# Optimization experiments

Measured on AMD Instinct MI355X. Metric: run time of the kernel, lower is better.

Reference implementation:

```python
import jax, jax.numpy as jnp
import numpy as np

# Model dims (match init_kwargs)
L, H, CV, NRBF = 4, 64, 16, 16   # layers, scalar hidden, vector channels (hidden/channels_div analog), radial basis size
HEADS, DH = 8, 8                 # num_heads, head dim (H // HEADS)
K = 32                           # k nearest neighbors
DIN = H + H + NRBF + CV + CV     # invariant edge-feature width = 176
N_ATOM_TYPES, ATOM_DIM, TIME_DIM, N_T = 32, 32, 32, 1000


def _sinusoidal(seq_len, dim):
    pos = np.arange(seq_len, dtype=np.float32)[:, None]
    dims = np.arange(dim, dtype=np.float32)[None, :]
    ang = pos / 10000 ** (2 * np.floor(dims / 2) / dim)
    emb = np.zeros((seq_len, dim), np.float32)
    emb[:, 0::2] = np.sin(ang[:, 0::2])
    emb[:, 1::2] = np.cos(ang[:, 1::2])
    return jnp.asarray(emb)


def _knn_idx(coord, k):
    # coord [b,n,3]; squared distances via gram trick (no [b,n,n,3] intermediate)
    sq = jnp.sum(coord * coord, axis=-1)
    d2 = sq[:, :, None] + sq[:, None, :] - 2.0 * jnp.einsum('bnd,bmd->bnm', coord, coord)
    n = coord.shape[1]
    d2 = d2 + jnp.eye(n, dtype=coord.dtype) * 1e9  # exclude self-loops
    _, idx = jax.lax.top_k(-d2, k)
    return idx  # [b,n,k] source-node indices for each destination node


_gather = jax.vmap(lambda x, i: x[i])  # ([n,...],[n,k]) -> [n,k,...], vmapped over batch


def _rbf(d, rmax=10.0):
    mu = jnp.linspace(0.0, rmax, NRBF)
    sigma = rmax / NRBF
    return jnp.exp(-((d[..., None] - mu) ** 2) / (2.0 * sigma * sigma))


def setup_inputs():
    key = jax.random.key(0)
    ks = jax.random.split(key, 16)
    b, n = 2, 2048

    def w(k, shape, scale):
        return jax.random.normal(k, shape, jnp.float32) * scale

    s = 1.0 / np.sqrt(H)
    return {
        'sequence': jax.random.randint(ks[0], (b, n), 0, N_ATOM_TYPES),
        'coordinate': jax.random.normal(ks[1], (b, n, 3), jnp.float32) * 3.0,
        't': 500,
        'atom_table': w(ks[2], (N_ATOM_TYPES, ATOM_DIM), 1.0),
        'time_table': _sinusoidal(N_T, TIME_DIM),
        'Wp0': w(ks[3], (ATOM_DIM + TIME_DIM, H), 1.0 / np.sqrt(ATOM_DIM + TIME_DIM)),
        'bp0': jnp.zeros((H,), jnp.float32),
        'Wp1': w(ks[4], (CV,), 1.0),
        'We1': w(ks[5], (L, DIN, H), 1.0 / np.sqrt(DIN)),
        'be1': jnp.zeros((L, H), jnp.float32),
        'We2': w(ks[6], (L, H, H), s),
        'be2': jnp.zeros((L, H), jnp.float32),
        'Wq': w(ks[7], (L, H, H), s),
        'Wk': w(ks[8], (L, H, H), s),
        'Wv0': w(ks[9], (L, H, H), s),
        'Wv1': w(ks[10], (L, H, CV), s),
        'Wg1': w(ks[11], (L, H, CV), s),
        'Wo0': w(ks[12], (L, H, H), s),
        'bo0': jnp.zeros((L, H), jnp.float32),
        'Wout1': w(ks[13], (CV,), 1.0 / np.sqrt(CV)),
    }


def reference(sequence, coordinate, t, atom_table, time_table, Wp0, bp0, Wp1,
              We1, be1, We2, be2, Wq, Wk, Wv0, Wv1, Wg1, Wo0, bo0, Wout1):
    b, n, _ = coordinate.shape
    coord = coordinate - jnp.mean(coordinate, axis=1, keepdims=True)

    # KNN graph + per-edge relative positions (src - dst), dense [b,n,K] layout
    idx = _knn_idx(coord, K)
    rel = _gather(coord, idx) - coord[:, :, None, :]      # [b,n,K,3]
    d = jnp.sqrt(jnp.sum(rel * rel, axis=-1) + 1e-8)
    dirn = rel / d[..., None]                             # degree-1 spherical harmonic direction
    rbf = _rbf(d)                                         # [b,n,K,NRBF]

    # input fibers: degree-0 = atom embedding ++ timestep embedding; degree-1 = coordinates
    f0 = jnp.concatenate([atom_table[sequence],
                          jnp.broadcast_to(time_table[t], (b, n, TIME_DIM))], axis=-1)
    f0 = f0 @ Wp0 + bp0                                   # [b,n,H]
    f1 = coord[:, :, None, :] * Wp1[None, None, :, None]  # [b,n,CV,3]

    for l in range(L):
        f0s = _gather(f0, idx)                            # [b,n,K,H] source scalars
        f1s = _gather(f1, idx)                            # [b,n,K,CV,3] source vectors
        dot_s = jnp.einsum('bnkcd,bnkd->bnkc', f1s, dirn) # invariants <f1_src, dir>
        dot_d = jnp.einsum('bncd,bnkd->bnkc', f1, dirn)   # invariants <f1_dst, dir>
        e = jnp.concatenate([jnp.broadcast_to(f0[:, :, None, :], f0s.shape),
                             f0s, rbf, dot_s, dot_d], axis=-1)
        m = jax.nn.relu(e @ We1[l] + be1[l]) @ We2[l] + be2[l]   # [b,n,K,H]

        # multi-head attention over the K neighbors
        q = (f0 @ Wq[l]).reshape(b, n, HEADS, DH)
        kk = (m @ Wk[l]).reshape(b, n, K, HEADS, DH)
        logits = jnp.einsum('bnhd,bnkhd->bnkh', q, kk) / np.sqrt(DH)
        attn = jax.nn.softmax(logits, axis=2)

        v0 = (m @ Wv0[l]).reshape(b, n, K, HEADS, DH)
        agg0 = jnp.einsum('bnkh,bnkhd->bnhd', attn, v0).reshape(b, n, H)
        f0 = f0 + agg0 @ Wo0[l] + bo0[l]

        # equivariant degree-1 update: dir-outer-product + gated source vectors
        a = attn.mean(axis=-1)                            # [b,n,K]
        v1 = dirn[..., None, :] * (m @ Wv1[l])[..., None] + (m @ Wg1[l])[..., None] * f1s
        f1 = f1 + jnp.einsum('bnk,bnkcd->bncd', a, v1)

    # output fiber: single degree-1 channel -> updated coordinates
    return jnp.einsum('bncd,c->bnd', f1, Wout1)           # [b,n,3]
```

## Files before the change

### kernel.cpp

```cpp
#include <hip/hip_runtime.h>
#include <hip/hip_bf16.h>
#include <math.h>

#define NL    4
#define H     64
#define CV    16
#define NRBF  16
#define HEADS 8
#define KK    32
#define DIN   176
#define NB    2
#define NN    2048
#define F1W   (CV*3)
#define NTILES 136

typedef __attribute__((ext_vector_type(8))) short short8v;
typedef __attribute__((ext_vector_type(4))) float floatx4;

__device__ __forceinline__ ushort f2bf(float f) {
  union { float f; unsigned u; } v; v.f = f;
  unsigned r = v.u + 0x7FFFu + ((v.u >> 16) & 1u);
  return (ushort)(r >> 16);
}
__device__ __forceinline__ float bf2f(ushort s) {
  union { unsigned u; float f; } v; v.u = ((unsigned)s) << 16;
  return v.f;
}
__device__ __forceinline__ void split_bf(float v, ushort& h, ushort& l) {
  h = f2bf(v);
  l = f2bf(v - bf2f(h));
}
__device__ __forceinline__ floatx4 mfma3(short8v ah, short8v al,
                                         short8v bh, short8v bl, floatx4 acc) {
  acc = __builtin_amdgcn_mfma_f32_16x16x32_bf16(ah, bh, acc, 0, 0, 0);
  acc = __builtin_amdgcn_mfma_f32_16x16x32_bf16(ah, bl, acc, 0, 0, 0);
  acc = __builtin_amdgcn_mfma_f32_16x16x32_bf16(al, bh, acc, 0, 0, 0);
  return acc;
}

__global__ __launch_bounds__(256) void k_center(const float* __restrict__ coord,
                                                float* __restrict__ coordC) {
  __shared__ float rx[256], ry[256], rz[256];
  int b = blockIdx.x;
  const float* cb = coord + b*NN*3;
  float sx = 0.f, sy = 0.f, sz = 0.f;
  for (int i = threadIdx.x; i < NN; i += 256) {
    sx += cb[i*3+0]; sy += cb[i*3+1]; sz += cb[i*3+2];
  }
  rx[threadIdx.x] = sx; ry[threadIdx.x] = sy; rz[threadIdx.x] = sz;
  __syncthreads();
  for (int s = 128; s > 0; s >>= 1) {
    if (threadIdx.x < s) {
      rx[threadIdx.x] += rx[threadIdx.x+s];
      ry[threadIdx.x] += ry[threadIdx.x+s];
      rz[threadIdx.x] += rz[threadIdx.x+s];
    }
    __syncthreads();
  }
  float mx = rx[0]*(1.0f/NN), my = ry[0]*(1.0f/NN), mz = rz[0]*(1.0f/NN);
  float* ob = coordC + b*NN*3;
  for (int i = threadIdx.x; i < NN; i += 256) {
    ob[i*3+0] = cb[i*3+0] - mx;
    ob[i*3+1] = cb[i*3+1] - my;
    ob[i*3+2] = cb[i*3+2] - mz;
  }
}

__global__ __launch_bounds__(64) void k_knn(const float* __restrict__ coordC,
                                            int* __restrict__ idx,
                                            float* __restrict__ dirn,
                                            ushort* __restrict__ rbf16) {
  __shared__ unsigned long long heap[64*33];
  const int node = blockIdx.x;
  const int b = node >> 11;
  const int i = node & (NN-1);
  const int l = threadIdx.x;
  const float* cb = coordC + b*NN*3;
  const float xi = cb[i*3+0], yi = cb[i*3+1], zi = cb[i*3+2];
  const float sqi = xi*xi + yi*yi + zi*zi;
  unsigned long long key[32];
  #pragma unroll
  for (int it = 0; it < 32; ++it) {
    int j = it*64 + l;
    float xj = cb[j*3+0], yj = cb[j*3+1], zj = cb[j*3+2];
    float sqj = xj*xj + yj*yj + zj*zj;
    float dot = xi*xj + yi*yj + zi*zj;
    float v = sqi + sqj - 2.0f*dot;
    if (j == i) v += 1.0e9f;
    unsigned u = __float_as_uint(v);
    u ^= (u >> 31) ? 0xFFFFFFFFu : 0x80000000u;
    key[it] = (((unsigned long long)u) << 16) | (unsigned)j;
  }
  #pragma unroll
  for (int k2 = 2; k2 <= 32; k2 <<= 1) {
    #pragma unroll
    for (int jj = k2 >> 1; jj > 0; jj >>= 1) {
      #pragma unroll
      for (int ii = 0; ii < 32; ++ii) {
        int ixj = ii ^ jj;
        if (ixj > ii) {
          bool up = ((ii & k2) == 0);
          unsigned long long a = key[ii], c = key[ixj];
          bool sw = (a > c) == up;
          unsigned long long lo = sw ? c : a;
          unsigned long long hi = sw ? a : c;
          key[ii] = lo; key[ixj] = hi;
        }
      }
    }
  }
  unsigned long long* row = heap + l*33;
  #pragma unroll
  for (int it = 0; it < 32; ++it) row[it] = key[it];
  row[32] = 0xFFFFFFFFFFFFFFFFULL;
  int ptr = 0;
  unsigned long long head = key[0];
  int myselidx = 0;
  for (int s = 0; s < KK; ++s) {
    unsigned long long w = head;
    #pragma unroll
    for (int off = 1; off <= 32; off <<= 1) {
      unsigned long long o = __shfl_xor(w, off, 64);
      w = (o < w) ? o : w;
    }
    int wj = (int)(w & 0xFFFFull);
    if (l == s) myselidx = wj;
    if ((wj & 63) == l) { ++ptr; head = row[ptr]; }
  }
  if (l < KK) {
    int j = myselidx;
    idx[node*KK + l] = j;
    float rxv = cb[j*3+0] - xi, ryv = cb[j*3+1] - yi, rzv = cb[j*3+2] - zi;
    float dd = sqrtf(rxv*rxv + ryv*ryv + rzv*rzv + 1e-8f);
    float inv = 1.0f/dd;
    float* dn = dirn + (node*KK + l)*3;
    dn[0] = rxv*inv; dn[1] = ryv*inv; dn[2] = rzv*inv;
    ushort* rb = rbf16 + (size_t)(node*KK + l)*NRBF;
    const float inv2s2 = 1.0f/(2.0f*0.625f*0.625f);
    #pragma unroll
    for (int r = 0; r < NRBF; ++r) {
      float mu = (10.0f/15.0f)*(float)r;
      float dm = dd - mu;
      rb[r] = f2bf(expf(-(dm*dm)*inv2s2));
    }
  }
}

__global__ __launch_bounds__(256) void k_f0init(const int* __restrict__ seq,
                                                const int* __restrict__ tptr,
                                                const float* __restrict__ atab,
                                                const float* __restrict__ ttab,
                                                const float* __restrict__ Wp0,
                                                const float* __restrict__ bp0,
                                                float* __restrict__ f0) {
  int gidx = blockIdx.x*256 + threadIdx.x;
  int node = gidx >> 6, o = gidx & (H-1);
  int s = seq[node];
  int tv = tptr[0];
  const float* ar = atab + s*32;
  const float* tr = ttab + tv*32;
  float acc = bp0[o];
  for (int i2 = 0; i2 < 32; ++i2) acc = fmaf(ar[i2], Wp0[i2*H + o], acc);
  for (int i2 = 0; i2 < 32; ++i2) acc = fmaf(tr[i2], Wp0[(32+i2)*H + o], acc);
  f0[gidx] = acc;
}

__global__ __launch_bounds__(256) void k_f1init(const float* __restrict__ coordC,
                                                const float* __restrict__ Wp1,
                                                float* __restrict__ f1) {
  int gidx = blockIdx.x*256 + threadIdx.x;
  if (gidx >= NB*NN*F1W) return;
  int node = gidx / F1W;
  int r = gidx - node*F1W;
  int c = r / 3, d = r - c*3;
  f1[gidx] = coordC[node*3 + d] * Wp1[c];
}

__global__ __launch_bounds__(256) void k_prep(
    const float* __restrict__ We1, const float* __restrict__ We2,
    const float* __restrict__ Wq,  const float* __restrict__ Wk,
    const float* __restrict__ Wv0, const float* __restrict__ Wv1,
    const float* __restrict__ Wg1, const float* __restrict__ Wo0,
    ushort* __restrict__ wfrag) {
  int gid = blockIdx.x*256 + threadIdx.x;
  if (gid >= NL*NTILES*64) return;
  int lane = gid & 63;
  int tile = gid >> 6;
  int l = tile / NTILES;
  int tt = tile - l*NTILES;
  int part = (tt >= 68) ? 1 : 0;
  int t = part ? (tt - 68) : tt;
  int kt, nt, K = H;
  const float* src = nullptr;
  int wvg = 0;
  if (t < 24)      { kt = t>>2;           nt = t&3; src = We1 + (size_t)l*DIN*H; K = DIN; }
  else if (t < 32) { int u=t-24; kt=u>>2; nt = u&3; src = We2 + (size_t)l*H*H; }
  else if (t < 40) { int u=t-32; kt=u>>2; nt = u&3; src = Wk  + (size_t)l*H*H; }
  else if (t < 48) { int u=t-40; kt=u>>2; nt = u&3; src = Wq  + (size_t)l*H*H; }
  else if (t < 56) { int u=t-48; kt=u>>2; nt = u&3; src = Wv0 + (size_t)l*H*H; }
  else if (t < 60) { int u=t-56; kt=u>>1; nt = u&1; wvg = 1; }
  else             { int u=t-60; kt=u>>2; nt = u&3; src = Wo0 + (size_t)l*H*H; }
  ushort out[8];
  #pragma unroll
  for (int j = 0; j < 8; ++j) {
    int k = kt*32 + (lane>>4)*8 + j;
    int col = nt*16 + (lane&15);
    float v = 0.f;
    if (k < K) {
      if (wvg) v = (col < CV) ? Wv1[(size_t)l*H*CV + k*CV + col]
                              : Wg1[(size_t)l*H*CV + k*CV + (col-CV)];
      else     v = src[(size_t)k*H + col];
    }
    ushort h, lo; split_bf(v, h, lo);
    out[j] = part ? lo : h;
  }
  *(short8v*)(wfrag + (size_t)tile*512 + lane*8) = *(const short8v*)out;
}

__global__ __launch_bounds__(128) void k_layer(
    const float* __restrict__ f0i, const float* __restrict__ f1i,
    float* __restrict__ f0o, float* __restrict__ f1o,
    const int* __restrict__ idx, const float* __restrict__ dirn,
    const ushort* __restrict__ rbf16,
    const ushort* __restrict__ wfl,
    const float* __restrict__ be1, const float* __restrict__ be2,
    const float* __restrict__ bo0)
{
  __shared__ __align__(16) ushort regionA  [32*72];
  __shared__ __align__(16) ushort regionAlo[32*72];
  __shared__ __align__(16) ushort regionB  [32*72];
  __shared__ __align__(16) ushort regionBlo[32*72];
  __shared__ __align__(16) ushort sF0h[64], sF0l[64];
  __shared__ __align__(16) ushort sAggH[64], sAggL[64];
  __shared__ float sF1d[F1W];
  __shared__ float sDir[KK][4];
  __shared__ int   sIdx[KK];
  __shared__ float sAtt[KK*9];
  __shared__ float sA[KK];
  __shared__ float sQ[64];
  __shared__ float sAggP[2][64];

  const int t    = threadIdx.x;
  const int wid  = t >> 6;
  const int lane = t & 63;
  const int node = blockIdx.x;
  const int bbase = node & ~(NN-1);
  const int r0 = lane & 15, g = lane >> 4;
  const int mrow = wid*16 + r0;
  const floatx4 fz = {0.f, 0.f, 0.f, 0.f};

  short8v cbh[4], cbl[4];
  #pragma unroll
  for (int nt = 0; nt < 4; ++nt) {
    cbh[nt] = *(const short8v*)&wfl[(size_t)(nt)*512 + lane*8];
    cbl[nt] = *(const short8v*)&wfl[(size_t)(68 + nt)*512 + lane*8];
  }

  float f0reg = 0.f;
  if (wid == 0) {
    f0reg = f0i[node*H + lane];
    ushort h, l; split_bf(f0reg, h, l); sF0h[lane] = h; sF0l[lane] = l;
  } else {
    if (lane < KK)  sIdx[lane] = idx[node*KK + lane];
    if (lane < F1W) sF1d[lane] = f1i[node*F1W + lane];
  }
  if (t < 96) sDir[t/3][t%3] = dirn[node*(KK*3) + t];
  __syncthreads();

  #pragma unroll 4
  for (int r = 0; r < 16; ++r) {
    int rr = wid*16 + r;
    float v = f0i[(bbase + sIdx[rr])*H + lane];
    ushort h, l; split_bf(v, h, l);
    regionA[rr*72 + lane] = h; regionAlo[rr*72 + lane] = l;
  }
  #pragma unroll
  for (int it = 0; it < 4; ++it) {
    int q = it*64 + lane;
    int k = wid*16 + (q >> 4), c = q & 15;
    regionB  [k*72 + c] = rbf16[(size_t)node*(KK*NRBF) + k*NRBF + c];
    regionBlo[k*72 + c] = 0;
    regionB  [k*72 + 48 + c] = 0;
    regionBlo[k*72 + 48 + c] = 0;
  }
  #pragma unroll
  for (int it = 0; it < 4; ++it) {
    int q = it*64 + lane;
    int k = wid*16 + (q >> 4), ch = q & 15;
    const float* fs = f1i + (size_t)(bbase + sIdx[k])*F1W + ch*3;
    float ds_ = 0.f, dd_ = 0.f;
    #pragma unroll
    for (int d = 0; d < 3; ++d) {
      float dr = sDir[k][d];
      ds_ += fs[d] * dr;
      dd_ += sF1d[ch*3 + d] * dr;
    }
    ushort h, l;
    split_bf(ds_, h, l); regionB[k*72 + 16 + ch] = h; regionBlo[k*72 + 16 + ch] = l;
    split_bf(dd_, h, l); regionB[k*72 + 32 + ch] = h; regionBlo[k*72 + 32 + ch] = l;
  }

  floatx4 c1[4];
  #pragma unroll
  for (int nt = 0; nt < 4; ++nt) c1[nt] = fz;
  #pragma unroll
  for (int kt = 0; kt < 6; ++kt) {
    short8v nbh[4], nbl[4];
    if (kt < 5) {
      #pragma unroll
      for (int nt = 0; nt < 4; ++nt) {
        nbh[nt] = *(const short8v*)&wfl[(size_t)((kt+1)*4 + nt)*512 + lane*8];
        nbl[nt] = *(const short8v*)&wfl[(size_t)(68 + (kt+1)*4 + nt)*512 + lane*8];
      }
    }
    short8v ah, al;
    if (kt < 2) {
      ah = *(const short8v*)&sF0h[kt*32 + g*8];
      al = *(const short8v*)&sF0l[kt*32 + g*8];
    } else if (kt < 4) {
      int off = (kt-2)*32 + g*8;
      ah = *(const short8v*)&regionA  [mrow*72 + off];
      al = *(const short8v*)&regionAlo[mrow*72 + off];
    } else {
      int off = ((kt == 4) ? 0 : 32) + g*8;
      ah = *(const short8v*)&regionB  [mrow*72 + off];
      al = *(const short8v*)&regionBlo[mrow*72 + off];
    }
    #pragma unroll
    for (int nt = 0; nt < 4; ++nt) c1[nt] = mfma3(ah, al, cbh[nt], cbl[nt], c1[nt]);
    if (kt < 5) {
      #pragma unroll
      for (int nt = 0; nt < 4; ++nt) { cbh[nt] = nbh[nt]; cbl[nt] = nbl[nt]; }
    }
  }
  short8v b2h[8], b2l[8];
  #pragma unroll
  for (int i2 = 0; i2 < 8; ++i2) {
    b2h[i2] = *(const short8v*)&wfl[(size_t)(24 + i2)*512 + lane*8];
    b2l[i2] = *(const short8v*)&wfl[(size_t)(92 + i2)*512 + lane*8];
  }
  #pragma unroll
  for (int nt = 0; nt < 4; ++nt) {
    float be = be1[nt*16 + r0];
    #pragma unroll
    for (int i = 0; i < 4; ++i) {
      float v = fmaxf(c1[nt][i] + be, 0.f);
      ushort h, l; split_bf(v, h, l);
      regionA  [(wid*16 + g*4 + i)*72 + nt*16 + r0] = h;
      regionAlo[(wid*16 + g*4 + i)*72 + nt*16 + r0] = l;
    }
  }

  floatx4 c2[4];
  #pragma unroll
  for (int nt = 0; nt < 4; ++nt) c2[nt] = fz;
  #pragma unroll
  for (int kt = 0; kt < 2; ++kt) {
    int off = kt*32 + g*8;
    short8v ah = *(const short8v*)&regionA  [mrow*72 + off];
    short8v al = *(const short8v*)&regionAlo[mrow*72 + off];
    #pragma unroll
    for (int nt = 0; nt < 4; ++nt)
      c2[nt] = mfma3(ah, al, b2h[kt*4 + nt], b2l[kt*4 + nt], c2[nt]);
  }
  #pragma unroll
  for (int nt = 0; nt < 4; ++nt) {
    float be = be2[nt*16 + r0];
    #pragma unroll
    for (int i = 0; i < 4; ++i) {
      ushort h, l; split_bf(c2[nt][i] + be, h, l);
      regionB  [(wid*16 + g*4 + i)*72 + nt*16 + r0] = h;
      regionBlo[(wid*16 + g*4 + i)*72 + nt*16 + r0] = l;
    }
  }

  floatx4 ck[4];
  #pragma unroll
  for (int nt = 0; nt < 4; ++nt) ck[nt] = fz;
  if (wid == 0) {
    floatx4 cq[4];
    #pragma unroll
    for (int nt = 0; nt < 4; ++nt) cq[nt] = fz;
    #pragma unroll
    for (int kt = 0; kt < 2; ++kt) {
      short8v ah = *(const short8v*)&sF0h[kt*32 + g*8];
      short8v al = *(const short8v*)&sF0l[kt*32 + g*8];
      #pragma unroll
      for (int nt = 0; nt < 4; ++nt) {
        short8v bh = *(const short8v*)&wfl[(size_t)(40 + kt*4 + nt)*512 + lane*8];
        short8v bl = *(const short8v*)&wfl[(size_t)(108 + kt*4 + nt)*512 + lane*8];
        cq[nt] = mfma3(ah, al, bh, bl, cq[nt]);
      }
    }
    if (g == 0) {
      #pragma unroll
      for (int nt = 0; nt < 4; ++nt) sQ[nt*16 + r0] = cq[nt][0];
    }
  } else {
    #pragma unroll
    for (int kt = 0; kt < 2; ++kt) {
      int off = kt*32 + g*8;
      short8v ah = *(const short8v*)&regionB  [mrow*72 + off];
      short8v al = *(const short8v*)&regionBlo[mrow*72 + off];
      #pragma unroll
      for (int nt = 0; nt < 4; ++nt) {
        short8v bh = *(const short8v*)&wfl[(size_t)(32 + kt*4 + nt)*512 + lane*8];
        short8v bl = *(const short8v*)&wfl[(size_t)(100 + kt*4 + nt)*512 + lane*8];
        ck[nt] = mfma3(ah, al, bh, bl, ck[nt]);
      }
    }
  }
  __syncthreads();

  floatx4 cv[4];
  #pragma unroll
  for (int nt = 0; nt < 4; ++nt) cv[nt] = fz;
  if (wid == 0) {
    #pragma unroll
    for (int kt = 0; kt < 2; ++kt) {
      int off = kt*32 + g*8;
      short8v ah = *(const short8v*)&regionB  [mrow*72 + off];
      short8v al = *(const short8v*)&regionBlo[mrow*72 + off];
      #pragma unroll
      for (int nt = 0; nt < 4; ++nt) {
        short8v bh = *(const short8v*)&wfl[(size_t)(32 + kt*4 + nt)*512 + lane*8];
        short8v bl = *(const short8v*)&wfl[(size_t)(100 + kt*4 + nt)*512 + lane*8];
        ck[nt] = mfma3(ah, al, bh, bl, ck[nt]);
      }
    }
  } else {
    #pragma unroll
    for (int kt = 0; kt < 2; ++kt) {
      int off = kt*32 + g*8;
      short8v ah = *(const short8v*)&regionB  [mrow*72 + off];
      short8v al = *(const short8v*)&regionBlo[mrow*72 + off];
      #pragma unroll
      for (int nt = 0; nt < 4; ++nt) {
        short8v bh = *(const short8v*)&wfl[(size_t)(48 + kt*4 + nt)*512 + lane*8];
        short8v bl = *(const short8v*)&wfl[(size_t)(116 + kt*4 + nt)*512 + lane*8];
        cv[nt] = mfma3(ah, al, bh, bl, cv[nt]);
      }
    }
  }
  {
    float qv[4];
    #pragma unroll
    for (int nt = 0; nt < 4; ++nt) qv[nt] = sQ[nt*16 + r0];
    #pragma unroll
    for (int nt = 0; nt < 4; ++nt)
      #pragma unroll
      for (int i = 0; i < 4; ++i) {
        float v = ck[nt][i] * qv[nt];
        v += __shfl_xor(v, 1, 64);
        v += __shfl_xor(v, 2, 64);
        v += __shfl_xor(v, 4, 64);
        if ((lane & 7) == 0)
          sAtt[(wid*16 + g*4 + i)*9 + nt*2 + (r0 >> 3)] = v * 0.35355339059327373f;
      }
  }
  __syncthreads();

  floatx4 cvg[2];
  cvg[0] = fz; cvg[1] = fz;
  if (wid == 1) {
    int h = lane & 7, seg = lane >> 3;
    float l0[4];
    float mx = -3.0e38f;
    #pragma unroll
    for (int i = 0; i < 4; ++i) { l0[i] = sAtt[(seg*4 + i)*9 + h]; mx = fmaxf(mx, l0[i]); }
    #pragma unroll
    for (int off = 8; off <= 32; off <<= 1) mx = fmaxf(mx, __shfl_xor(mx, off, 64));
    float e0[4], sum = 0.f;
    #pragma unroll
    for (int i = 0; i < 4; ++i) { e0[i] = expf(l0[i] - mx); sum += e0[i]; }
    #pragma unroll
    for (int off = 8; off <= 32; off <<= 1) sum += __shfl_xor(sum, off, 64);
    float inv = 1.0f / sum;
    #pragma unroll
    for (int i = 0; i < 4; ++i) {
      float a = e0[i] * inv;
      sAtt[(seg*4 + i)*9 + h] = a;
      float tt = a;
      tt += __shfl_xor(tt, 1, 64);
      tt += __shfl_xor(tt, 2, 64);
      tt += __shfl_xor(tt, 4, 64);
      if (h == 0) sA[seg*4 + i] = tt * 0.125f;
    }
  } else {
    #pragma unroll
    for (int kt = 0; kt < 2; ++kt) {
      int off = kt*32 + g*8;
      short8v ah = *(const short8v*)&regionB  [mrow*72 + off];
      short8v al = *(const short8v*)&regionBlo[mrow*72 + off];
      #pragma unroll
      for (int nt = 0; nt < 4; ++nt) {
        short8v bh = *(const short8v*)&wfl[(size_t)(48 + kt*4 + nt)*512 + lane*8];
        short8v bl = *(const short8v*)&wfl[(size_t)(116 + kt*4 + nt)*512 + lane*8];
        cv[nt] = mfma3(ah, al, bh, bl, cv[nt]);
      }
      #pragma unroll
      for (int nt = 0; nt < 2; ++nt) {
        short8v bh = *(const short8v*)&wfl[(size_t)(56 + kt*2 + nt)*512 + lane*8];
        short8v bl = *(const short8v*)&wfl[(size_t)(124 + kt*2 + nt)*512 + lane*8];
        cvg[nt] = mfma3(ah, al, bh, bl, cvg[nt]);
      }
    }
    float* sMvg = (float*)regionA;
    #pragma unroll
    for (int nt = 0; nt < 2; ++nt)
      #pragma unroll
      for (int i = 0; i < 4; ++i)
        sMvg[(g*4 + i)*34 + nt*16 + r0] = cvg[nt][i];
  }
  __syncthreads();

  short8v b7h[8], b7l[8];
  if (wid == 0) {
    #pragma unroll
    for (int i2 = 0; i2 < 8; ++i2) {
      b7h[i2] = *(const short8v*)&wfl[(size_t)(60 + i2)*512 + lane*8];
      b7l[i2] = *(const short8v*)&wfl[(size_t)(128 + i2)*512 + lane*8];
    }
  }
  {
    int hsub = r0 >> 3;
    #pragma unroll
    for (int nt = 0; nt < 4; ++nt) {
      float p = 0.f;
      #pragma unroll
      for (int i = 0; i < 4; ++i)
        p += sAtt[(wid*16 + g*4 + i)*9 + nt*2 + hsub] * cv[nt][i];
      p += __shfl_xor(p, 16, 64);
      p += __shfl_xor(p, 32, 64);
      if (g == 0) sAggP[wid][nt*16 + r0] = p;
    }
  }
  if (wid == 1) {
    cvg[0] = fz; cvg[1] = fz;
    #pragma unroll
    for (int kt = 0; kt < 2; ++kt) {
      int off = kt*32 + g*8;
      short8v ah = *(const short8v*)&regionB  [mrow*72 + off];
      short8v al = *(const short8v*)&regionBlo[mrow*72 + off];
      #pragma unroll
      for (int nt = 0; nt < 2; ++nt) {
        short8v bh = *(const short8v*)&wfl[(size_t)(56 + kt*2 + nt)*512 + lane*8];
        short8v bl = *(const short8v*)&wfl[(size_t)(124 + kt*2 + nt)*512 + lane*8];
        cvg[nt] = mfma3(ah, al, bh, bl, cvg[nt]);
      }
    }
    float* sMvg = (float*)regionA;
    #pragma unroll
    for (int nt = 0; nt < 2; ++nt)
      #pragma unroll
      for (int i = 0; i < 4; ++i)
        sMvg[(16 + g*4 + i)*34 + nt*16 + r0] = cvg[nt][i];
  }
  __syncthreads();

  if (wid == 0) {
    {
      float p = sAggP[0][lane] + sAggP[1][lane];
      ushort h, l; split_bf(p, h, l);
      sAggH[lane] = h; sAggL[lane] = l;
    }
    floatx4 co[4];
    #pragma unroll
    for (int nt = 0; nt < 4; ++nt) co[nt] = fz;
    #pragma unroll
    for (int kt = 0; kt < 2; ++kt) {
      short8v ah = *(const short8v*)&sAggH[kt*32 + g*8];
      short8v al = *(const short8v*)&sAggL[kt*32 + g*8];
      #pragma unroll
      for (int nt = 0; nt < 4; ++nt)
        co[nt] = mfma3(ah, al, b7h[kt*4 + nt], b7l[kt*4 + nt], co[nt]);
    }
    float v = (g == 0) ? co[0][0] : (g == 1) ? co[1][0] : (g == 2) ? co[2][0] : co[3][0];
    f0o[node*H + lane] = f0reg + v + bo0[lane];
  } else if (lane < F1W) {
    const float* sMvg = (const float*)regionA;
    int ch = lane / 3, d = lane - ch*3;
    float acc = sF1d[lane];
    #pragma unroll 8
    for (int k = 0; k < KK; ++k) {
      float f1s = f1i[(size_t)(bbase + sIdx[k])*F1W + lane];
      float a   = sA[k];
      float mv1 = sMvg[k*34 + ch];
      float mg1 = sMvg[k*34 + 16 + ch];
      acc += a * (sDir[k][d]*mv1 + mg1*f1s);
    }
    f1o[node*F1W + lane] = acc;
  }
}

__global__ __launch_bounds__(256) void k_out(const float* __restrict__ f1,
                                             const float* __restrict__ Wout1,
                                             float* __restrict__ out) {
  int gidx = blockIdx.x*256 + threadIdx.x;
  if (gidx >= NB*NN*3) return;
  int node = gidx / 3, d = gidx - node*3;
  float acc = 0.f;
  for (int c = 0; c < CV; ++c) acc = fmaf(f1[node*F1W + c*3 + d], Wout1[c], acc);
  out[gidx] = acc;
}

extern "C" void kernel_launch(void* const* d_in, const int* in_sizes, int n_in,
                              void* d_out, int out_size, void* d_ws, size_t ws_size,
                              hipStream_t stream) {
  const int*   seq   = (const int*)  d_in[0];
  const float* coord = (const float*)d_in[1];
  const int*   tptr  = (const int*)  d_in[2];
  const float* atab  = (const float*)d_in[3];
  const float* ttab  = (const float*)d_in[4];
  const float* Wp0   = (const float*)d_in[5];
  const float* bp0   = (const float*)d_in[6];
  const float* Wp1   = (const float*)d_in[7];
  const float* We1   = (const float*)d_in[8];
  const float* be1   = (const float*)d_in[9];
  const float* We2   = (const float*)d_in[10];
  const float* be2   = (const float*)d_in[11];
  const float* Wq    = (const float*)d_in[12];
  const float* Wk    = (const float*)d_in[13];
  const float* Wv0   = (const float*)d_in[14];
  const float* Wv1   = (const float*)d_in[15];
  const float* Wg1   = (const float*)d_in[16];
  const float* Wo0   = (const float*)d_in[17];
  const float* bo0   = (const float*)d_in[18];
  const float* Wout1 = (const float*)d_in[19];
  float* out = (float*)d_out;

  float* ws = (float*)d_ws;
  float*  coordC = ws;
  int*    idxb   = (int*)(ws + 12288);
  float*  dirn   = ws + 12288 + 131072;
  float*  f0A    = dirn + (size_t)NB*NN*KK*3;
  float*  f0B    = f0A + (size_t)NB*NN*H;
  float*  f1A    = f0B + (size_t)NB*NN*H;
  float*  f1B    = f1A + (size_t)NB*NN*F1W;
  ushort* rbf16  = (ushort*)(f1B + (size_t)NB*NN*F1W);
  ushort* wfrag  = rbf16 + (size_t)NB*NN*KK*NRBF;

  k_center<<<NB, 256, 0, stream>>>(coord, coordC);
  k_knn<<<NB*NN, 64, 0, stream>>>(coordC, idxb, dirn, rbf16);
  k_f0init<<<NB*NN*H/256, 256, 0, stream>>>(seq, tptr, atab, ttab, Wp0, bp0, f0A);
  k_f1init<<<(NB*NN*F1W + 255)/256, 256, 0, stream>>>(coordC, Wp1, f1A);
  k_prep<<<(NL*NTILES*64 + 255)/256, 256, 0, stream>>>(We1, We2, Wq, Wk, Wv0, Wv1, Wg1, Wo0, wfrag);

  const float* f0in = f0A; float* f0out = f0B;
  const float* f1in = f1A; float* f1out = f1B;
  for (int l = 0; l < NL; ++l) {
    k_layer<<<NB*NN, 128, 0, stream>>>(
        f0in, f1in, f0out, f1out, idxb, dirn, rbf16,
        wfrag + (size_t)l*NTILES*512,
        be1 + (size_t)l*H, be2 + (size_t)l*H, bo0 + (size_t)l*H);
    const float* tf0 = f0in; f0in = f0out; f0out = (float*)tf0;
    const float* tf1 = f1in; f1in = f1out; f1out = (float*)tf1;
  }
  k_out<<<(NB*NN*3 + 255)/256, 256, 0, stream>>>(f1in, Wout1, out);
}
```

Measured before the change: 368.9 us.

## Split per-node layer kernel across four waves with N-split MFMA tiles

Raises k_layer from 128 to 256 threads. Each wave now owns a 16-row M tile and half of the N tiles, so weight fragments are loaded per use instead of being held in registers. Softmax is spread across all waves with per-head 32-lane reductions and a partial-sum array for head-mean attention. The aim is more parallelism per node and lower register pressure. In exchange the kernel adds several extra __syncthreads and reloads weight fragments from global/L2 more often.

```diff
diff --git a/kernel.cpp b/kernel.cpp
--- a/kernel.cpp
+++ b/kernel.cpp
@@ -217,7 +217,7 @@
   *(short8v*)(wfrag + (size_t)tile*512 + lane*8) = *(const short8v*)out;
 }
 
-__global__ __launch_bounds__(128) void k_layer(
+__global__ __launch_bounds__(256, 6) void k_layer(
     const float* __restrict__ f0i, const float* __restrict__ f1i,
     float* __restrict__ f0o, float* __restrict__ f1o,
     const int* __restrict__ idx, const float* __restrict__ dirn,
@@ -239,54 +239,56 @@
   __shared__ float sA[KK];
   __shared__ float sQ[64];
   __shared__ float sAggP[2][64];
+  __shared__ float sAPart[4][32];
 
   const int t    = threadIdx.x;
   const int wid  = t >> 6;
   const int lane = t & 63;
+  const int mt   = wid >> 1;
+  const int nh   = wid & 1;
   const int node = blockIdx.x;
   const int bbase = node & ~(NN-1);
   const int r0 = lane & 15, g = lane >> 4;
-  const int mrow = wid*16 + r0;
+  const int mrow = mt*16 + r0;
   const floatx4 fz = {0.f, 0.f, 0.f, 0.f};
-
-  short8v cbh[4], cbl[4];
-  #pragma unroll
-  for (int nt = 0; nt < 4; ++nt) {
-    cbh[nt] = *(const short8v*)&wfl[(size_t)(nt)*512 + lane*8];
-    cbl[nt] = *(const short8v*)&wfl[(size_t)(68 + nt)*512 + lane*8];
-  }
 
   float f0reg = 0.f;
   if (wid == 0) {
     f0reg = f0i[node*H + lane];
     ushort h, l; split_bf(f0reg, h, l); sF0h[lane] = h; sF0l[lane] = l;
+  } else if (wid == 1) {
+    if (lane < KK) sIdx[lane] = idx[node*KK + lane];
+  } else if (wid == 2) {
+    if (lane < F1W) sF1d[lane] = f1i[node*F1W + lane];
   } else {
-    if (lane < KK)  sIdx[lane] = idx[node*KK + lane];
-    if (lane < F1W) sF1d[lane] = f1i[node*F1W + lane];
-  }
-  if (t < 96) sDir[t/3][t%3] = dirn[node*(KK*3) + t];
-  __syncthreads();
-
-  #pragma unroll 4
-  for (int r = 0; r < 16; ++r) {
-    int rr = wid*16 + r;
+    sDir[lane/3][lane%3] = dirn[node*(KK*3) + lane];
+    if (lane < 32) {
+      int e = 64 + lane;
+      sDir[e/3][e%3] = dirn[node*(KK*3) + e];
+    }
+  }
+  __syncthreads();
+
+  #pragma unroll
+  for (int r = 0; r < 8; ++r) {
+    int rr = wid*8 + r;
     float v = f0i[(bbase + sIdx[rr])*H + lane];
     ushort h, l; split_bf(v, h, l);
     regionA[rr*72 + lane] = h; regionAlo[rr*72 + lane] = l;
   }
   #pragma unroll
-  for (int it = 0; it < 4; ++it) {
-    int q = it*64 + lane;
-    int k = wid*16 + (q >> 4), c = q & 15;
-    regionB  [k*72 + c] = rbf16[(size_t)node*(KK*NRBF) + k*NRBF + c];
+  for (int it = 0; it < 2; ++it) {
+    int p = it*256 + t;
+    int k = p >> 4, c = p & 15;
+    regionB  [k*72 + c] = rbf16[(size_t)node*(KK*NRBF) + p];
     regionBlo[k*72 + c] = 0;
     regionB  [k*72 + 48 + c] = 0;
     regionBlo[k*72 + 48 + c] = 0;
   }
   #pragma unroll
-  for (int it = 0; it < 4; ++it) {
-    int q = it*64 + lane;
-    int k = wid*16 + (q >> 4), ch = q & 15;
+  for (int it = 0; it < 2; ++it) {
+    int p = it*256 + t;
+    int k = p >> 4, ch = p & 15;
     const float* fs = f1i + (size_t)(bbase + sIdx[k])*F1W + ch*3;
     float ds_ = 0.f, dd_ = 0.f;
     #pragma unroll
@@ -299,20 +301,11 @@
     split_bf(ds_, h, l); regionB[k*72 + 16 + ch] = h; regionBlo[k*72 + 16 + ch] = l;
     split_bf(dd_, h, l); regionB[k*72 + 32 + ch] = h; regionBlo[k*72 + 32 + ch] = l;
   }
-
-  floatx4 c1[4];
-  #pragma unroll
-  for (int nt = 0; nt < 4; ++nt) c1[nt] = fz;
+  __syncthreads();
+
+  floatx4 c1[2]; c1[0] = fz; c1[1] = fz;
   #pragma unroll
   for (int kt = 0; kt < 6; ++kt) {
-    short8v nbh[4], nbl[4];
-    if (kt < 5) {
-      #pragma unroll
-      for (int nt = 0; nt < 4; ++nt) {
-        nbh[nt] = *(const short8v*)&wfl[(size_t)((kt+1)*4 + nt)*512 + lane*8];
-        nbl[nt] = *(const short8v*)&wfl[(size_t)(68 + (kt+1)*4 + nt)*512 + lane*8];
-      }
-    }
     short8v ah, al;
     if (kt < 2) {
       ah = *(const short8v*)&sF0h[kt*32 + g*8];
@@ -327,74 +320,87 @@
       al = *(const short8v*)&regionBlo[mrow*72 + off];
     }
     #pragma unroll
-    for (int nt = 0; nt < 4; ++nt) c1[nt] = mfma3(ah, al, cbh[nt], cbl[nt], c1[nt]);
-    if (kt < 5) {
-      #pragma unroll
-      for (int nt = 0; nt < 4; ++nt) { cbh[nt] = nbh[nt]; cbl[nt] = nbl[nt]; }
-    }
-  }
-  short8v b2h[8], b2l[8];
-  #pragma unroll
-  for (int i2 = 0; i2 < 8; ++i2) {
-    b2h[i2] = *(const short8v*)&wfl[(size_t)(24 + i2)*512 + lane*8];
-    b2l[i2] = *(const short8v*)&wfl[(size_t)(92 + i2)*512 + lane*8];
-  }
-  #pragma unroll
-  for (int nt = 0; nt < 4; ++nt) {
-    float be = be1[nt*16 + r0];
+    for (int j = 0; j < 2; ++j) {
+      int ntg = nh*2 + j;
+      short8v bh = *(const short8v*)&wfl[(size_t)(kt*4 + ntg)*512 + lane*8];
+      short8v bl = *(const short8v*)&wfl[(size_t)(68 + kt*4 + ntg)*512 + lane*8];
+      c1[j] = mfma3(ah, al, bh, bl, c1[j]);
+    }
+  }
+  #pragma unroll
+  for (int j = 0; j < 2; ++j) {
+    int ntg = nh*2 + j;
+    float be = be1[ntg*16 + r0];
     #pragma unroll
     for (int i = 0; i < 4; ++i) {
-      float v = fmaxf(c1[nt][i] + be, 0.f);
+      float v = fmaxf(c1[j][i] + be, 0.f);
       ushort h, l; split_bf(v, h, l);
-      regionA  [(wid*16 + g*4 + i)*72 + nt*16 + r0] = h;
-      regionAlo[(wid*16 + g*4 + i)*72 + nt*16 + r0] = l;
-    }
-  }
-
-  floatx4 c2[4];
-  #pragma unroll
-  for (int nt = 0; nt < 4; ++nt) c2[nt] = fz;
+      regionA  [(mt*16 + g*4 + i)*72 + ntg*16 + r0] = h;
+      regionAlo[(mt*16 + g*4 + i)*72 + ntg*16 + r0] = l;
+    }
+  }
+  __syncthreads();
+
+  floatx4 c2[2]; c2[0] = fz; c2[1] = fz;
   #pragma unroll
   for (int kt = 0; kt < 2; ++kt) {
     int off = kt*32 + g*8;
     short8v ah = *(const short8v*)&regionA  [mrow*72 + off];
     short8v al = *(const short8v*)&regionAlo[mrow*72 + off];
     #pragma unroll
-    for (int nt = 0; nt < 4; ++nt)
-      c2[nt] = mfma3(ah, al, b2h[kt*4 + nt], b2l[kt*4 + nt], c2[nt]);
-  }
-  #pragma unroll
-  for (int nt = 0; nt < 4; ++nt) {
-    float be = be2[nt*16 + r0];
+    for (int j = 0; j < 2; ++j) {
+      int ntg = nh*2 + j;
+      short8v bh = *(const short8v*)&wfl[(size_t)(24 + kt*4 + ntg)*512 + lane*8];
+      short8v bl = *(const short8v*)&wfl[(size_t)(92 + kt*4 + ntg)*512 + lane*8];
+      c2[j] = mfma3(ah, al, bh, bl, c2[j]);
+    }
+  }
+  __syncthreads();
+  #pragma unroll
+  for (int j = 0; j < 2; ++j) {
+    int ntg = nh*2 + j;
+    float be = be2[ntg*16 + r0];
     #pragma unroll
     for (int i = 0; i < 4; ++i) {
-      ushort h, l; split_bf(c2[nt][i] + be, h, l);
-      regionB  [(wid*16 + g*4 + i)*72 + nt*16 + r0] = h;
-      regionBlo[(wid*16 + g*4 + i)*72 + nt*16 + r0] = l;
-    }
-  }
-
-  floatx4 ck[4];
-  #pragma unroll
-  for (int nt = 0; nt < 4; ++nt) ck[nt] = fz;
-  if (wid == 0) {
-    floatx4 cq[4];
-    #pragma unroll
-    for (int nt = 0; nt < 4; ++nt) cq[nt] = fz;
+      ushort h, l; split_bf(c2[j][i] + be, h, l);
+      regionB  [(mt*16 + g*4 + i)*72 + ntg*16 + r0] = h;
+      regionBlo[(mt*16 + g*4 + i)*72 + ntg*16 + r0] = l;
+    }
+  }
+  __syncthreads();
+
+  floatx4 ck[2]; ck[0] = fz; ck[1] = fz;
+  floatx4 cv[2]; cv[0] = fz; cv[1] = fz;
+  #pragma unroll
+  for (int kt = 0; kt < 2; ++kt) {
+    int off = kt*32 + g*8;
+    short8v ah = *(const short8v*)&regionB  [mrow*72 + off];
+    short8v al = *(const short8v*)&regionBlo[mrow*72 + off];
+    #pragma unroll
+    for (int j = 0; j < 2; ++j) {
+      int ntg = nh*2 + j;
+      short8v bh = *(const short8v*)&wfl[(size_t)(32 + kt*4 + ntg)*512 + lane*8];
+      short8v bl = *(const short8v*)&wfl[(size_t)(100 + kt*4 + ntg)*512 + lane*8];
+      ck[j] = mfma3(ah, al, bh, bl, ck[j]);
+    }
+  }
+  if (mt == 0) {
+    floatx4 cq[2]; cq[0] = fz; cq[1] = fz;
     #pragma unroll
     for (int kt = 0; kt < 2; ++kt) {
       short8v ah = *(const short8v*)&sF0h[kt*32 + g*8];
       short8v al = *(const short8v*)&sF0l[kt*32 + g*8];
       #pragma unroll
-      for (int nt = 0; nt < 4; ++nt) {
-        short8v bh = *(const short8v*)&wfl[(size_t)(40 + kt*4 + nt)*512 + lane*8];
-        short8v bl = *(const short8v*)&wfl[(size_t)(108 + kt*4 + nt)*512 + lane*8];
-        cq[nt] = mfma3(ah, al, bh, bl, cq[nt]);
+      for (int j = 0; j < 2; ++j) {
+        int ntg = nh*2 + j;
+        short8v bh = *(const short8v*)&wfl[(size_t)(40 + kt*4 + ntg)*512 + lane*8];
+        short8v bl = *(const short8v*)&wfl[(size_t)(108 + kt*4 + ntg)*512 + lane*8];
+        cq[j] = mfma3(ah, al, bh, bl, cq[j]);
       }
     }
     if (g == 0) {
-      #pragma unroll
-      for (int nt = 0; nt < 4; ++nt) sQ[nt*16 + r0] = cq[nt][0];
+      sQ[(nh*2 + 0)*16 + r0] = cq[0][0];
+      sQ[(nh*2 + 1)*16 + r0] = cq[1][0];
     }
   } else {
     #pragma unroll
@@ -403,159 +409,99 @@
       short8v ah = *(const short8v*)&regionB  [mrow*72 + off];
       short8v al = *(const short8v*)&regionBlo[mrow*72 + off];
       #pragma unroll
-      for (int nt = 0; nt < 4; ++nt) {
-        short8v bh = *(const short8v*)&wfl[(size_t)(32 + kt*4 + nt)*512 + lane*8];
-        short8v bl = *(const short8v*)&wfl[(size_t)(100 + kt*4 + nt)*512 + lane*8];
-        ck[nt] = mfma3(ah, al, bh, bl, ck[nt]);
+      for (int j = 0; j < 2; ++j) {
+        int ntg = nh*2 + j;
+        short8v bh = *(const short8v*)&wfl[(size_t)(48 + kt*4 + ntg)*512 + lane*8];
+        short8v bl = *(const short8v*)&wfl[(size_t)(116 + kt*4 + ntg)*512 + lane*8];
+        cv[j] = mfma3(ah, al, bh, bl, cv[j]);
       }
     }
   }
   __syncthreads();
 
-  floatx4 cv[4];
-  #pragma unroll
-  for (int nt = 0; nt < 4; ++nt) cv[nt] = fz;
-  if (wid == 0) {
+  #pragma unroll
+  for (int j = 0; j < 2; ++j) {
+    int ntg = nh*2 + j;
+    float qv = sQ[ntg*16 + r0];
+    #pragma unroll
+    for (int i = 0; i < 4; ++i) {
+      float v = ck[j][i] * qv;
+      v += __shfl_xor(v, 1, 64);
+      v += __shfl_xor(v, 2, 64);
+      v += __shfl_xor(v, 4, 64);
+      if ((lane & 7) == 0)
+        sAtt[(mt*16 + g*4 + i)*9 + ntg*2 + (r0 >> 3)] = v * 0.35355339059327373f;
+    }
+  }
+  if (mt == 0) {
     #pragma unroll
     for (int kt = 0; kt < 2; ++kt) {
       int off = kt*32 + g*8;
       short8v ah = *(const short8v*)&regionB  [mrow*72 + off];
       short8v al = *(const short8v*)&regionBlo[mrow*72 + off];
       #pragma unroll
-      for (int nt = 0; nt < 4; ++nt) {
-        short8v bh = *(const short8v*)&wfl[(size_t)(32 + kt*4 + nt)*512 + lane*8];
-        short8v bl = *(const short8v*)&wfl[(size_t)(100 + kt*4 + nt)*512 + lane*8];
-        ck[nt] = mfma3(ah, al, bh, bl, ck[nt]);
+      for (int j = 0; j < 2; ++j) {
+        int ntg = nh*2 + j;
+        short8v bh = *(const short8v*)&wfl[(size_t)(48 + kt*4 + ntg)*512 + lane*8];
+        short8v bl = *(const short8v*)&wfl[(size_t)(116 + kt*4 + ntg)*512 + lane*8];
+        cv[j] = mfma3(ah, al, bh, bl, cv[j]);
       }
     }
   } else {
-    #pragma unroll
-    for (int kt = 0; kt < 2; ++kt) {
-      int off = kt*32 + g*8;
-      short8v ah = *(const short8v*)&regionB  [mrow*72 + off];
-      short8v al = *(const short8v*)&regionBlo[mrow*72 + off];
-      #pragma unroll
-      for (int nt = 0; nt < 4; ++nt) {
-        short8v bh = *(const short8v*)&wfl[(size_t)(48 + kt*4 + nt)*512 + lane*8];
-        short8v bl = *(const short8v*)&wfl[(size_t)(116 + kt*4 + nt)*512 + lane*8];
-        cv[nt] = mfma3(ah, al, bh, bl, cv[nt]);
+    float* sMvg = (float*)regionA;
+    #pragma unroll
+    for (int msub = 0; msub < 2; ++msub) {
+      floatx4 cvg = fz;
+      #pragma unroll
+      for (int kt = 0; kt < 2; ++kt) {
+        int off = kt*32 + g*8;
+        short8v ah = *(const short8v*)&regionB  [(msub*16 + r0)*72 + off];
+        short8v al = *(const short8v*)&regionBlo[(msub*16 + r0)*72 + off];
+        short8v bh = *(const short8v*)&wfl[(size_t)(56 + kt*2 + nh)*512 + lane*8];
+        short8v bl = *(const short8v*)&wfl[(size_t)(124 + kt*2 + nh)*512 + lane*8];
+        cvg = mfma3(ah, al, bh, bl, cvg);
       }
-    }
-  }
+      #pragma unroll
+      for (int i = 0; i < 4; ++i)
+        sMvg[(msub*16 + g*4 + i)*34 + nh*16 + r0] = cvg[i];
+    }
+  }
+  __syncthreads();
+
   {
-    float qv[4];
-    #pragma unroll
-    for (int nt = 0; nt < 4; ++nt) qv[nt] = sQ[nt*16 + r0];
-    #pragma unroll
-    for (int nt = 0; nt < 4; ++nt)
-      #pragma unroll
-      for (int i = 0; i < 4; ++i) {
-        float v = ck[nt][i] * qv[nt];
-        v += __shfl_xor(v, 1, 64);
-        v += __shfl_xor(v, 2, 64);
-        v += __shfl_xor(v, 4, 64);
-        if ((lane & 7) == 0)
-          sAtt[(wid*16 + g*4 + i)*9 + nt*2 + (r0 >> 3)] = v * 0.35355339059327373f;
-      }
-  }
-  __syncthreads();
-
-  floatx4 cvg[2];
-  cvg[0] = fz; cvg[1] = fz;
-  if (wid == 1) {
-    int h = lane & 7, seg = lane >> 3;
-    float l0[4];
-    float mx = -3.0e38f;
-    #pragma unroll
-    for (int i = 0; i < 4; ++i) { l0[i] = sAtt[(seg*4 + i)*9 + h]; mx = fmaxf(mx, l0[i]); }
-    #pragma unroll
-    for (int off = 8; off <= 32; off <<= 1) mx = fmaxf(mx, __shfl_xor(mx, off, 64));
-    float e0[4], sum = 0.f;
-    #pragma unroll
-    for (int i = 0; i < 4; ++i) { e0[i] = expf(l0[i] - mx); sum += e0[i]; }
-    #pragma unroll
-    for (int off = 8; off <= 32; off <<= 1) sum += __shfl_xor(sum, off, 64);
-    float inv = 1.0f / sum;
-    #pragma unroll
-    for (int i = 0; i < 4; ++i) {
-      float a = e0[i] * inv;
-      sAtt[(seg*4 + i)*9 + h] = a;
-      float tt = a;
-      tt += __shfl_xor(tt, 1, 64);
-      tt += __shfl_xor(tt, 2, 64);
-      tt += __shfl_xor(tt, 4, 64);
-      if (h == 0) sA[seg*4 + i] = tt * 0.125f;
-    }
-  } else {
-    #pragma unroll
-    for (int kt = 0; kt < 2; ++kt) {
-      int off = kt*32 + g*8;
-      short8v ah = *(const short8v*)&regionB  [mrow*72 + off];
-      short8v al = *(const short8v*)&regionBlo[mrow*72 + off];
-      #pragma unroll
-      for (int nt = 0; nt < 4; ++nt) {
-        short8v bh = *(const short8v*)&wfl[(size_t)(48 + kt*4 + nt)*512 + lane*8];
-        short8v bl = *(const short8v*)&wfl[(size_t)(116 + kt*4 + nt)*512 + lane*8];
-        cv[nt] = mfma3(ah, al, bh, bl, cv[nt]);
-      }
-      #pragma unroll
-      for (int nt = 0; nt < 2; ++nt) {
-        short8v bh = *(const short8v*)&wfl[(size_t)(56 + kt*2 + nt)*512 + lane*8];
-        short8v bl = *(const short8v*)&wfl[(size_t)(124 + kt*2 + nt)*512 + lane*8];
-        cvg[nt] = mfma3(ah, al, bh, bl, cvg[nt]);
-      }
-    }
-    float* sMvg = (float*)regionA;
-    #pragma unroll
-    for (int nt = 0; nt < 2; ++nt)
+    int head = wid*2 + (lane >> 5);
+    int k = lane & 31;
+    float lg = sAtt[k*9 + head];
+    float mx = lg;
+    #pragma unroll
+    for (int off = 1; off <= 16; off <<= 1) mx = fmaxf(mx, __shfl_xor(mx, off, 64));
+    float e = expf(lg - mx);
+    float sum = e;
+    #pragma unroll
+    for (int off = 1; off <= 16; off <<= 1) sum += __shfl_xor(sum, off, 64);
+    float a = e / sum;
+    sAtt[k*9 + head] = a;
+    float pr = a + __shfl_xor(a, 32, 64);
+    if (lane < 32) sAPart[wid][k] = pr;
+  }
+  __syncthreads();
+
+  {
+    #pragma unroll
+    for (int j = 0; j < 2; ++j) {
+      int ntg = nh*2 + j;
+      int head = ntg*2 + (r0 >> 3);
+      float p = 0.f;
       #pragma unroll
       for (int i = 0; i < 4; ++i)
-        sMvg[(g*4 + i)*34 + nt*16 + r0] = cvg[nt][i];
-  }
-  __syncthreads();
-
-  short8v b7h[8], b7l[8];
-  if (wid == 0) {
-    #pragma unroll
-    for (int i2 = 0; i2 < 8; ++i2) {
-      b7h[i2] = *(const short8v*)&wfl[(size_t)(60 + i2)*512 + lane*8];
-      b7l[i2] = *(const short8v*)&wfl[(size_t)(128 + i2)*512 + lane*8];
-    }
-  }
-  {
-    int hsub = r0 >> 3;
-    #pragma unroll
-    for (int nt = 0; nt < 4; ++nt) {
-      float p = 0.f;
-      #pragma unroll
-      for (int i = 0; i < 4; ++i)
-        p += sAtt[(wid*16 + g*4 + i)*9 + nt*2 + hsub] * cv[nt][i];
+        p += sAtt[(mt*16 + g*4 + i)*9 + head] * cv[j][i];
       p += __shfl_xor(p, 16, 64);
       p += __shfl_xor(p, 32, 64);
-      if (g == 0) sAggP[wid][nt*16 + r0] = p;
-    }
-  }
-  if (wid == 1) {
-    cvg[0] = fz; cvg[1] = fz;
-    #pragma unroll
-    for (int kt = 0; kt < 2; ++kt) {
-      int off = kt*32 + g*8;
-      short8v ah = *(const short8v*)&regionB  [mrow*72 + off];
-      short8v al = *(const short8v*)&regionBlo[mrow*72 + off];
-      #pragma unroll
-      for (int nt = 0; nt < 2; ++nt) {
-        short8v bh = *(const short8v*)&wfl[(size_t)(56 + kt*2 + nt)*512 + lane*8];
-        short8v bl = *(const short8v*)&wfl[(size_t)(124 + kt*2 + nt)*512 + lane*8];
-        cvg[nt] = mfma3(ah, al, bh, bl, cvg[nt]);
-      }
-    }
-    float* sMvg = (float*)regionA;
-    #pragma unroll
-    for (int nt = 0; nt < 2; ++nt)
-      #pragma unroll
-      for (int i = 0; i < 4; ++i)
-        sMvg[(16 + g*4 + i)*34 + nt*16 + r0] = cvg[nt][i];
-  }
+      if (g == 0) sAggP[mt][ntg*16 + r0] = p;
+    }
+  }
+  if (wid == 3 && lane < 32)
+    sA[lane] = 0.125f*(sAPart[0][lane] + sAPart[1][lane] + sAPart[2][lane] + sAPart[3][lane]);
   __syncthreads();
 
   if (wid == 0) {
@@ -572,12 +518,15 @@
       short8v ah = *(const short8v*)&sAggH[kt*32 + g*8];
       short8v al = *(const short8v*)&sAggL[kt*32 + g*8];
       #pragma unroll
-      for (int nt = 0; nt < 4; ++nt)
-        co[nt] = mfma3(ah, al, b7h[kt*4 + nt], b7l[kt*4 + nt], co[nt]);
+      for (int nt = 0; nt < 4; ++nt) {
+        short8v bh = *(const short8v*)&wfl[(size_t)(60 + kt*4 + nt)*512 + lane*8];
+        short8v bl = *(const short8v*)&wfl[(size_t)(128 + kt*4 + nt)*512 + lane*8];
+        co[nt] = mfma3(ah, al, bh, bl, co[nt]);
+      }
     }
     float v = (g == 0) ? co[0][0] : (g == 1) ? co[1][0] : (g == 2) ? co[2][0] : co[3][0];
     f0o[node*H + lane] = f0reg + v + bo0[lane];
-  } else if (lane < F1W) {
+  } else if (wid == 1 && lane < F1W) {
     const float* sMvg = (const float*)regionA;
     int ch = lane / 3, d = lane - ch*3;
     float acc = sF1d[lane];
@@ -649,7 +598,7 @@
   const float* f0in = f0A; float* f0out = f0B;
   const float* f1in = f1A; float* f1out = f1B;
   for (int l = 0; l < NL; ++l) {
-    k_layer<<<NB*NN, 128, 0, stream>>>(
+    k_layer<<<NB*NN, 256, 0, stream>>>(
         f0in, f1in, f0out, f1out, idxb, dirn, rbf16,
         wfrag + (size_t)l*NTILES*512,
         be1 + (size_t)l*H, be2 + (size_t)l*H, bo0 + (size_t)l*H);
```

After: 328.1 us. 1.12x faster.
